# Kernel optimization log

Measured on AMD Instinct MI355X. Metric: run time of the kernel, lower is better.

The kernel has to match this reference:

```python
import jax, jax.numpy as jnp
from jax import lax
import numpy as np

HID = 100  # embedding_dim == hidden_dim == 100 (hardcoded in module)
VOCAB = 128000
NUM_CLASSES = 20
SEQ_LEN = 8192


def setup_inputs() -> dict:
    key = jax.random.key(0)
    ks = jax.random.split(key, 8)
    s = 1.0 / np.sqrt(HID)
    return {
        "sequence": jax.random.randint(ks[0], (SEQ_LEN,), 0, VOCAB, dtype=jnp.int64 if jax.config.jax_enable_x64 else jnp.int32),
        "embedding": jax.random.normal(ks[1], (VOCAB, HID), dtype=jnp.float32),
        "W_ih": jax.random.uniform(ks[2], (4 * HID, HID), minval=-s, maxval=s, dtype=jnp.float32),
        "W_hh": jax.random.uniform(ks[3], (4 * HID, HID), minval=-s, maxval=s, dtype=jnp.float32),
        "b_ih": jax.random.uniform(ks[4], (4 * HID,), minval=-s, maxval=s, dtype=jnp.float32),
        "b_hh": jax.random.uniform(ks[5], (4 * HID,), minval=-s, maxval=s, dtype=jnp.float32),
        "fc_w": jax.random.uniform(ks[6], (NUM_CLASSES, HID), minval=-s, maxval=s, dtype=jnp.float32),
        "fc_b": jax.random.uniform(ks[7], (NUM_CLASSES,), minval=-s, maxval=s, dtype=jnp.float32),
    }


def reference(sequence, embedding, W_ih, W_hh, b_ih, b_hh, fc_w, fc_b):
    # embeds: [N, HID] gather from embedding table
    embeds = embedding[sequence]
    # precompute input projections for all timesteps in one GEMM: [N, 4H]
    x_proj = embeds @ W_ih.T + b_ih + b_hh

    def step(carry, xp):
        h, c = carry  # [HID], [HID]
        gates = xp + W_hh @ h  # [4H]; PyTorch gate order i, f, g, o
        i, f, g, o = jnp.split(gates, 4)
        i = jax.nn.sigmoid(i)
        f = jax.nn.sigmoid(f)
        g = jnp.tanh(g)
        o = jax.nn.sigmoid(o)
        c = f * c + i * g
        h = o * jnp.tanh(c)
        return (h, c), None

    h0 = jnp.zeros((HID,), dtype=embeds.dtype)
    c0 = jnp.zeros((HID,), dtype=embeds.dtype)
    (h_last, _), _ = lax.scan(step, (h0, c0), x_proj)
    out = h_last @ fc_w.T + fc_b  # fc on final-timestep output
    return out[None, :]  # view(1, -1)
```

## Files before the change

### kernel.cpp

```cpp
#include <hip/hip_runtime.h>

#define SEQ  8192
#define HID  100
#define G4   400
#define NCLS 20

__device__ __forceinline__ float fast_sigmoid(float x) {
    return 1.0f / (1.0f + __expf(-x));
}
__device__ __forceinline__ float fast_tanh(float x) {
    float e = __expf(2.0f * x);
    return 1.0f - 2.0f / (e + 1.0f);
}

__device__ __forceinline__ void wg_barrier() {
    asm volatile("s_waitcnt lgkmcnt(0)" ::: "memory");
    __builtin_amdgcn_s_barrier();
    asm volatile("" ::: "memory");
}

__global__ __launch_bounds__(512)
void xproj_kernel(const int* __restrict__ seq, const float* __restrict__ emb,
                  const float* __restrict__ Wih, const float* __restrict__ bih,
                  const float* __restrict__ bhh, float* __restrict__ xp)
{
    __shared__ float er[8][HID];
    const int tid = threadIdx.x;
    const int t0  = blockIdx.x * 8;

    if (tid < 200) {
        int r = tid / 25, q = tid - r * 25;
        int s = seq[t0 + r];
        *(float4*)&er[r][4 * q] = *(const float4*)&emb[(size_t)s * HID + 4 * q];
    }
    __syncthreads();

    const int row = (tid < G4) ? tid : (G4 - 1);
    const float4* wr = (const float4*)(Wih + row * HID);
    const float bias = bih[row] + bhh[row];

    float acc[8];
    #pragma unroll
    for (int u = 0; u < 8; ++u) acc[u] = bias;

    #pragma unroll
    for (int k = 0; k < 25; ++k) {
        float4 wv = wr[k];
        #pragma unroll
        for (int u = 0; u < 8; ++u) {
            float4 ev = *(const float4*)&er[u][4 * k];
            acc[u] = fmaf(wv.x, ev.x, acc[u]);
            acc[u] = fmaf(wv.y, ev.y, acc[u]);
            acc[u] = fmaf(wv.z, ev.z, acc[u]);
            acc[u] = fmaf(wv.w, ev.w, acc[u]);
        }
    }
    if (tid < G4) {
        #pragma unroll
        for (int u = 0; u < 8; ++u)
            xp[(size_t)(t0 + u) * G4 + tid] = acc[u];
    }
}

template<int MODE>
__global__ __launch_bounds__(512, 2)
void lstm_scan(const float* __restrict__ xp,
               const float* __restrict__ Whh,
               const float* __restrict__ fcw, const float* __restrict__ fcb,
               const int* __restrict__ seq, const float* __restrict__ emb,
               const float* __restrict__ Wih, const float* __restrict__ bih,
               const float* __restrict__ bhh,
               float* __restrict__ out)
{
    __shared__ float h_s[128];
    __shared__ float g_s[G4];
    __shared__ float er_s[HID];

    const int tid = threadIdx.x;
    const int row = (tid < G4) ? tid : (G4 - 1);
    const int cls = row / HID;

    float4 w[25];
    {
        const float4* wr = (const float4*)(Whh + row * HID);
        #pragma unroll
        for (int k = 0; k < 25; ++k) w[k] = wr[k];
    }
    float bias2 = 0.0f;
    if constexpr (MODE == 1) bias2 = bih[row] + bhh[row];

    if (tid < 128) h_s[tid] = 0.0f;
    float c = 0.0f;

    float xn[8];
    if constexpr (MODE == 0) {
        #pragma unroll
        for (int u = 0; u < 8; ++u)
            xn[u] = (tid < G4) ? xp[u * G4 + tid] : 0.0f;
    }
    wg_barrier();

    #pragma unroll 1
    for (int t8 = 0; t8 < SEQ; t8 += 8) {
        #pragma unroll
        for (int u = 0; u < 8; ++u) {
            const int t = t8 + u;
            float xcur;
            if constexpr (MODE == 0) {
                xcur = xn[u];
                if (t8 + 8 < SEQ && tid < G4)
                    xn[u] = xp[(size_t)(t + 8) * G4 + tid];
            } else {
                int s = seq[t];
                if (tid < 25)
                    *(float4*)&er_s[4 * tid] =
                        *(const float4*)&emb[(size_t)s * HID + 4 * tid];
                wg_barrier();
                xcur = bias2;
                const float4* xr = (const float4*)(Wih + row * HID);
                #pragma unroll
                for (int k = 0; k < 25; ++k) {
                    float4 wv = xr[k];
                    float4 ev = *(const float4*)&er_s[4 * k];
                    xcur = fmaf(wv.x, ev.x, xcur);
                    xcur = fmaf(wv.y, ev.y, xcur);
                    xcur = fmaf(wv.z, ev.z, xcur);
                    xcur = fmaf(wv.w, ev.w, xcur);
                }
            }

            float2 a0 = make_float2(xcur, 0.0f);
            float2 a1 = make_float2(0.0f, 0.0f);
            #pragma unroll
            for (int k = 0; k < 25; ++k) {
                float4 hv = *(const float4*)&h_s[4 * k];
                a0.x = fmaf(w[k].x, hv.x, a0.x);
                a0.y = fmaf(w[k].y, hv.y, a0.y);
                a1.x = fmaf(w[k].z, hv.z, a1.x);
                a1.y = fmaf(w[k].w, hv.w, a1.y);
            }
            float acc = (a0.x + a1.x) + (a0.y + a1.y);

            float gv = (cls == 2) ? fast_tanh(acc) : fast_sigmoid(acc);
            if (tid < G4) g_s[tid] = gv;
            wg_barrier();

            if (tid < HID) {
                float gi = g_s[tid];
                float gf = g_s[tid + HID];
                float gg = g_s[tid + 2 * HID];
                float go = g_s[tid + 3 * HID];
                c = fmaf(gf, c, gi * gg);
                h_s[tid] = go * fast_tanh(c);
            }
            wg_barrier();
        }
    }

    if (tid < NCLS) {
        const float* fr = fcw + tid * HID;
        float s0 = fcb[tid];
        #pragma unroll
        for (int k = 0; k < HID; ++k) s0 = fmaf(fr[k], h_s[k], s0);
        out[tid] = s0;
    }
}

extern "C" void kernel_launch(void* const* d_in, const int* in_sizes, int n_in,
                              void* d_out, int out_size, void* d_ws, size_t ws_size,
                              hipStream_t stream)
{
    const int*   seq = (const int*)d_in[0];
    const float* emb = (const float*)d_in[1];
    const float* Wih = (const float*)d_in[2];
    const float* Whh = (const float*)d_in[3];
    const float* bih = (const float*)d_in[4];
    const float* bhh = (const float*)d_in[5];
    const float* fcw = (const float*)d_in[6];
    const float* fcb = (const float*)d_in[7];
    float* out = (float*)d_out;
    float* xp  = (float*)d_ws;

    const size_t need = (size_t)SEQ * G4 * sizeof(float);
    if (ws_size >= need) {
        xproj_kernel<<<SEQ / 8, 512, 0, stream>>>(seq, emb, Wih, bih, bhh, xp);
        lstm_scan<0><<<1, 512, 0, stream>>>(xp, Whh, fcw, fcb,
                                            seq, emb, Wih, bih, bhh, out);
    } else {
        lstm_scan<1><<<1, 512, 0, stream>>>(nullptr, Whh, fcw, fcb,
                                            seq, emb, Wih, bih, bhh, out);
    }
}
```

Baseline: 6.322 ms.

## Interleave LSTM gates per hidden unit, exchange via shuffles, double-buffer h

Reorders the gate rows so the four gates of each hidden unit sit in adjacent lanes. The xproj output is permuted to match, and gates are exchanged with lane shuffles instead of going through shared memory. This removes one of the two workgroup barriers per timestep and the gate shared array. h is double-buffered so the single remaining barrier is enough. The xproj kernel now processes 16 timesteps per block, and the dot product uses packed two-wide FMAs with four accumulators.

```diff
diff --git a/kernel.cpp b/kernel.cpp
--- a/kernel.cpp
+++ b/kernel.cpp
@@ -4,6 +4,9 @@
 #define HID  100
 #define G4   400
 #define NCLS 20
+
+typedef float v2f __attribute__((ext_vector_type(2)));
+typedef float v4f __attribute__((ext_vector_type(4)));
 
 __device__ __forceinline__ float fast_sigmoid(float x) {
     return 1.0f / (1.0f + __expf(-x));
@@ -24,11 +27,11 @@
                   const float* __restrict__ Wih, const float* __restrict__ bih,
                   const float* __restrict__ bhh, float* __restrict__ xp)
 {
-    __shared__ float er[8][HID];
+    __shared__ float er[16][HID];
     const int tid = threadIdx.x;
-    const int t0  = blockIdx.x * 8;
-
-    if (tid < 200) {
+    const int t0  = blockIdx.x * 16;
+
+    if (tid < 400) {
         int r = tid / 25, q = tid - r * 25;
         int s = seq[t0 + r];
         *(float4*)&er[r][4 * q] = *(const float4*)&emb[(size_t)s * HID + 4 * q];
@@ -36,18 +39,18 @@
     __syncthreads();
 
     const int row = (tid < G4) ? tid : (G4 - 1);
-    const float4* wr = (const float4*)(Wih + row * HID);
+    const float4* wr = (const float4*)(Wih + (size_t)row * HID);
     const float bias = bih[row] + bhh[row];
 
-    float acc[8];
+    float acc[16];
     #pragma unroll
-    for (int u = 0; u < 8; ++u) acc[u] = bias;
+    for (int u = 0; u < 16; ++u) acc[u] = bias;
 
     #pragma unroll
     for (int k = 0; k < 25; ++k) {
         float4 wv = wr[k];
         #pragma unroll
-        for (int u = 0; u < 8; ++u) {
+        for (int u = 0; u < 16; ++u) {
             float4 ev = *(const float4*)&er[u][4 * k];
             acc[u] = fmaf(wv.x, ev.x, acc[u]);
             acc[u] = fmaf(wv.y, ev.y, acc[u]);
@@ -56,40 +59,46 @@
         }
     }
     if (tid < G4) {
-        #pragma unroll
-        for (int u = 0; u < 8; ++u)
-            xp[(size_t)(t0 + u) * G4 + tid] = acc[u];
+        const int cj = row / HID, rj = row - cj * HID;
+        const int pj = rj * 4 + cj;
+        #pragma unroll
+        for (int u = 0; u < 16; ++u)
+            xp[(size_t)(t0 + u) * G4 + pj] = acc[u];
     }
 }
 
 template<int MODE>
 __global__ __launch_bounds__(512, 2)
-void lstm_scan(const float* __restrict__ xp,
+void lstm_scan(const float* xp,
                const float* __restrict__ Whh,
-               const float* __restrict__ fcw, const float* __restrict__ fcb,
+               const float* __restrict__ fcw,
+               const float* __restrict__ fcb,
                const int* __restrict__ seq, const float* __restrict__ emb,
                const float* __restrict__ Wih, const float* __restrict__ bih,
                const float* __restrict__ bhh,
                float* __restrict__ out)
 {
-    __shared__ float h_s[128];
-    __shared__ float g_s[G4];
+    __shared__ v4f  h4[2][32];
     __shared__ float er_s[HID];
 
     const int tid = threadIdx.x;
-    const int row = (tid < G4) ? tid : (G4 - 1);
-    const int cls = row / HID;
-
-    float4 w[25];
+    const int cls = tid & 3;
+    const int grp = tid >> 2;
+    const int row = (grp < HID) ? grp : (HID - 1);
+    const int grow = cls * HID + row;
+
+    v4f wv[25];
     {
-        const float4* wr = (const float4*)(Whh + row * HID);
-        #pragma unroll
-        for (int k = 0; k < 25; ++k) w[k] = wr[k];
+        const v4f* wr = (const v4f*)(Whh + (size_t)grow * HID);
+        #pragma unroll
+        for (int k = 0; k < 25; ++k) wv[k] = wr[k];
+        #pragma unroll
+        for (int k = 0; k < 25; ++k) asm volatile("" : "+v"(wv[k]));
     }
     float bias2 = 0.0f;
-    if constexpr (MODE == 1) bias2 = bih[row] + bhh[row];
-
-    if (tid < 128) h_s[tid] = 0.0f;
+    if constexpr (MODE == 1) bias2 = bih[grow] + bhh[grow];
+
+    if (tid < 128) ((float*)h4)[tid] = 0.0f;
     float c = 0.0f;
 
     float xn[8];
@@ -108,61 +117,69 @@
             float xcur;
             if constexpr (MODE == 0) {
                 xcur = xn[u];
-                if (t8 + 8 < SEQ && tid < G4)
+                if (t + 8 < SEQ && tid < G4)
                     xn[u] = xp[(size_t)(t + 8) * G4 + tid];
             } else {
-                int s = seq[t];
+                int s_ = seq[t];
                 if (tid < 25)
                     *(float4*)&er_s[4 * tid] =
-                        *(const float4*)&emb[(size_t)s * HID + 4 * tid];
+                        *(const float4*)&emb[(size_t)s_ * HID + 4 * tid];
                 wg_barrier();
                 xcur = bias2;
-                const float4* xr = (const float4*)(Wih + row * HID);
+                const float4* xr = (const float4*)(Wih + (size_t)grow * HID);
                 #pragma unroll
                 for (int k = 0; k < 25; ++k) {
-                    float4 wv = xr[k];
+                    float4 wq = xr[k];
                     float4 ev = *(const float4*)&er_s[4 * k];
-                    xcur = fmaf(wv.x, ev.x, xcur);
-                    xcur = fmaf(wv.y, ev.y, xcur);
-                    xcur = fmaf(wv.z, ev.z, xcur);
-                    xcur = fmaf(wv.w, ev.w, xcur);
+                    xcur = fmaf(wq.x, ev.x, xcur);
+                    xcur = fmaf(wq.y, ev.y, xcur);
+                    xcur = fmaf(wq.z, ev.z, xcur);
+                    xcur = fmaf(wq.w, ev.w, xcur);
                 }
             }
 
-            float2 a0 = make_float2(xcur, 0.0f);
-            float2 a1 = make_float2(0.0f, 0.0f);
+            const v4f* hb = h4[u & 1];
+            v2f s0 = {xcur, 0.0f}, s1 = {0.0f, 0.0f};
+            v2f s2 = {0.0f, 0.0f}, s3 = {0.0f, 0.0f};
             #pragma unroll
             for (int k = 0; k < 25; ++k) {
-                float4 hv = *(const float4*)&h_s[4 * k];
-                a0.x = fmaf(w[k].x, hv.x, a0.x);
-                a0.y = fmaf(w[k].y, hv.y, a0.y);
-                a1.x = fmaf(w[k].z, hv.z, a1.x);
-                a1.y = fmaf(w[k].w, hv.w, a1.y);
+                v4f hv = hb[k];
+                if (k & 1) {
+                    s2 = __builtin_elementwise_fma(wv[k].lo, hv.lo, s2);
+                    s3 = __builtin_elementwise_fma(wv[k].hi, hv.hi, s3);
+                } else {
+                    s0 = __builtin_elementwise_fma(wv[k].lo, hv.lo, s0);
+                    s1 = __builtin_elementwise_fma(wv[k].hi, hv.hi, s1);
+                }
             }
-            float acc = (a0.x + a1.x) + (a0.y + a1.y);
-
-            float gv = (cls == 2) ? fast_tanh(acc) : fast_sigmoid(acc);
-            if (tid < G4) g_s[tid] = gv;
-            wg_barrier();
-
-            if (tid < HID) {
-                float gi = g_s[tid];
-                float gf = g_s[tid + HID];
-                float gg = g_s[tid + 2 * HID];
-                float go = g_s[tid + 3 * HID];
-                c = fmaf(gf, c, gi * gg);
-                h_s[tid] = go * fast_tanh(c);
-            }
+            v2f sr = (s0 + s2) + (s1 + s3);
+            float acc = sr.x + sr.y;
+
+            float a = (cls == 2) ? fast_tanh(acc) : fast_sigmoid(acc);
+            float b = __shfl_xor(a, 1);
+            float xv = (cls & 1) ? b : a;
+            float yv = (cls & 1) ? a : b;
+            float x2 = __shfl_xor(xv, 2);
+            float y2 = __shfl_xor(yv, 2);
+            const bool hi = cls >= 2;
+            float gi = hi ? x2 : xv, gg = hi ? xv : x2;
+            float gf = hi ? y2 : yv, go = hi ? yv : y2;
+
+            c = fmaf(gf, c, gi * gg);
+            float hn = go * fast_tanh(c);
+            if (cls == 0 && grp < HID)
+                ((float*)h4[(u & 1) ^ 1])[row] = hn;
             wg_barrier();
         }
     }
 
     if (tid < NCLS) {
-        const float* fr = fcw + tid * HID;
-        float s0 = fcb[tid];
-        #pragma unroll
-        for (int k = 0; k < HID; ++k) s0 = fmaf(fr[k], h_s[k], s0);
-        out[tid] = s0;
+        const float* hf = (const float*)h4[0];
+        const float* fr = fcw + (size_t)tid * HID;
+        float s = fcb[tid];
+        #pragma unroll
+        for (int k = 0; k < HID; ++k) s = fmaf(fr[k], hf[k], s);
+        out[tid] = s;
     }
 }
 
@@ -183,7 +200,7 @@
 
     const size_t need = (size_t)SEQ * G4 * sizeof(float);
     if (ws_size >= need) {
-        xproj_kernel<<<SEQ / 8, 512, 0, stream>>>(seq, emb, Wih, bih, bhh, xp);
+        xproj_kernel<<<SEQ / 16, 512, 0, stream>>>(seq, emb, Wih, bih, bhh, xp);
         lstm_scan<0><<<1, 512, 0, stream>>>(xp, Whh, fcw, fcb,
                                             seq, emb, Wih, bih, bhh, out);
     } else {
```

Measured after the change: 5.881 ms. -7.0%, faster.
